# Performance work log

Measured on AMD Instinct MI355X. Metric: run time of the kernel, lower is better.

## Reference

```python
import jax, jax.numpy as jnp
import numpy as np

N = 20000          # skill_num (nodes)
D = 128            # skill_embed_dim
E = 640000         # edges (avg degree 32)
T = 12             # seq_len
L = 3              # gcn_layers
PRESERVE = 0.1     # residual preserve_ratio


def setup_inputs() -> dict:
    key = jax.random.key(0)
    ks = jax.random.split(key, 8)
    demand_seq_emb = jax.random.normal(ks[0], (N, T, D), jnp.float32)
    supply_seq_emb = jax.random.normal(ks[1], (N, T, D), jnp.float32)
    edge_index = jax.random.randint(ks[2], (2, E), 0, N, dtype=jnp.int32)
    edge_attr = jax.random.uniform(ks[3], (E,), jnp.float32)
    emb_weight = jax.random.normal(ks[4], (N, D), jnp.float32) * 0.02
    fuse_W = jax.random.normal(ks[5], (D, 3 * D), jnp.float32) * (1.0 / np.sqrt(3 * D))
    fuse_b = jnp.zeros((D,), jnp.float32)
    gcn_W = jax.random.normal(ks[6], (L, D, D), jnp.float32) * (1.0 / np.sqrt(D))
    gcn_b = jnp.zeros((L, D), jnp.float32)
    return {
        "demand_seq_emb": demand_seq_emb,
        "supply_seq_emb": supply_seq_emb,
        "l": T, "t_s": 0, "t_e": T,                 # unused by forward (placeholders)
        "edge_index": edge_index,
        "edge_attr": edge_attr,
        "comm": 0, "skill_semantic_embed": 0, "init_emb": 0,  # unused placeholders
        "emb_weight": emb_weight,
        "fuse_W": fuse_W, "fuse_b": fuse_b,
        "gcn_W": gcn_W, "gcn_b": gcn_b,
    }


def _gcn_norm(src, dst, edge_w, n):
    """PyG gcn_norm with self-loops: norm_e = d^-1/2[src] * w_e * d^-1/2[dst]."""
    loop = jnp.arange(n, dtype=src.dtype)
    src2 = jnp.concatenate([src, loop])
    dst2 = jnp.concatenate([dst, loop])
    w2 = jnp.concatenate([edge_w, jnp.ones((n,), edge_w.dtype)])
    deg = jax.ops.segment_sum(w2, dst2, num_segments=n)
    dinv = jnp.where(deg > 0, jax.lax.rsqrt(deg), 0.0)
    norm = dinv[src2] * w2 * dinv[dst2]
    return src2, dst2, norm


def reference(demand_seq_emb, supply_seq_emb, l, t_s, t_e, edge_index, edge_attr,
              comm, skill_semantic_embed, init_emb,
              emb_weight, fuse_W, fuse_b, gcn_W, gcn_b):
    # fuse static embedding with last-step demand/supply sequence embeddings
    seq_last = jnp.concatenate([demand_seq_emb[:, -1, :], supply_seq_emb[:, -1, :]], axis=-1)  # [N,2D]
    fused = jnp.concatenate([emb_weight, seq_last], axis=-1) @ fuse_W.T + fuse_b  # [N,D]

    # edges are generated with all indices < skill_num, so the torch-side
    # `(edge_index < skill_num).all(0)` filter is the identity here.
    src, dst = edge_index[0], edge_index[1]
    src2, dst2, norm = _gcn_norm(src, dst, edge_attr, N)

    temp = fused
    for i in range(L):  # small fixed layer count
        x = temp @ gcn_W[i].T                                   # [N,D] linear (bias added post-agg)
        msg = norm[:, None] * x[src2]                           # gather + scale
        out = jax.ops.segment_sum(msg, dst2, num_segments=N) + gcn_b[i]  # scatter-add
        temp = (1.0 - PRESERVE) * out + PRESERVE * temp         # residual blend
    return temp  # skill_embs [N, D]
```

## Files before the change

### kernel.cpp

```cpp
#include <hip/hip_runtime.h>
#include <hip/hip_fp16.h>

#define NN 20000
#define DD 128
#define EE 640000
#define TSEQ 12
#define CAP 128

__device__ __forceinline__ void fma4(float4& acc, float a, const float4& w) {
  acc.x += a * w.x; acc.y += a * w.y; acc.z += a * w.z; acc.w += a * w.w;
}

__device__ __forceinline__ float4 h8_to_f4(uint2 v) {
  union { unsigned u; __half2 h; } a, b;
  a.u = v.x; b.u = v.y;
  float2 fa = __half22float2(a.h);
  float2 fb = __half22float2(b.h);
  return make_float4(fa.x, fa.y, fb.x, fb.y);
}

__device__ __forceinline__ uint2 f4_to_h8(float4 o) {
  union { unsigned u; __half2 h; } a, b;
  a.h = __floats2half2_rn(o.x, o.y);
  b.h = __floats2half2_rn(o.z, o.w);
  uint2 r; r.x = a.u; r.y = b.u;
  return r;
}

__global__ void k_init(float* __restrict__ deg, int* __restrict__ cnt) {
  int i = blockIdx.x * blockDim.x + threadIdx.x;
  if (i < NN) { deg[i] = 1.0f; cnt[i] = 0; }
}

__global__ void k_edge(const int* __restrict__ src, const int* __restrict__ dst,
                       const float* __restrict__ w,
                       float* __restrict__ deg, int* __restrict__ cnt,
                       uint2* __restrict__ csr) {
  int e = blockIdx.x * blockDim.x + threadIdx.x;
  if (e < EE) {
    int s = src[e], d = dst[e];
    float we = w[e];
    atomicAdd(&deg[d], we);
    int slot = atomicAdd(&cnt[d], 1);
    if (slot < CAP) csr[(size_t)d * CAP + slot] = make_uint2((unsigned)s, __float_as_uint(we));
  }
}

__global__ void k_transpose_all(const float* __restrict__ fuse_W,
                                const float* __restrict__ gcn_W,
                                float* __restrict__ fuse_Wt,
                                float* __restrict__ gWt0,
                                __half* __restrict__ gWh) {
  int i = blockIdx.x * blockDim.x + threadIdx.x;
  if (i < 49152) {
    int k = i >> 7, d = i & 127;
    fuse_Wt[i] = fuse_W[d * 384 + k];
  } else if (i < 65536) {
    int j = i - 49152;
    int k = j >> 7, d = j & 127;
    gWt0[j] = gcn_W[d * 128 + k];
  } else if (i < 98304) {
    int j = i - 65536;
    int l = 1 + (j >> 14), jj = j & 16383;
    int k = jj >> 7, d = jj & 127;
    gWh[j] = (__half)gcn_W[l * 16384 + d * 128 + k];
  }
}

#define G_TN 2
#define G_BN 32

__global__ __launch_bounds__(256, 4) void k_gemm(
    const float* __restrict__ a0, int s0,
    const float* __restrict__ a1, int s1,
    const float* __restrict__ a2, int s2,
    int nparts,
    const float* __restrict__ Wt,
    const float* __restrict__ bias,
    const float* __restrict__ deg_pm,
    float* __restrict__ outf,
    uint2* __restrict__ outh)
{
  __shared__ float Ws[64 * 128];
  const int t = threadIdx.x;
  const int dq = t & 15;
  const int ng = t >> 4;
  const int n_base = blockIdx.x * G_BN + ng * G_TN;

  float4 acc0[G_TN], acc1[G_TN];
  #pragma unroll
  for (int i = 0; i < G_TN; ++i) {
    acc0[i] = make_float4(0.f, 0.f, 0.f, 0.f);
    acc1[i] = make_float4(0.f, 0.f, 0.f, 0.f);
  }

  for (int p = 0; p < nparts; ++p) {
    const float* ap; int as;
    if (p == 0) { ap = a0; as = s0; }
    else if (p == 1) { ap = a1; as = s1; }
    else { ap = a2; as = s2; }
    const float* rp[G_TN];
    #pragma unroll
    for (int i = 0; i < G_TN; ++i) {
      int r = n_base + i; if (r >= NN) r = NN - 1;
      rp[i] = ap + (size_t)r * as;
    }

    for (int c = 0; c < 2; ++c) {
      const float4* wsrc = (const float4*)(Wt + (p * 128 + c * 64) * 128);
      float4* wdst = (float4*)Ws;
      #pragma unroll
      for (int it = 0; it < 8; ++it) wdst[it * 256 + t] = wsrc[it * 256 + t];
      __syncthreads();

      const int ks = c * 64;
      for (int k = 0; k < 64; k += 4) {
        float4 av[G_TN];
        #pragma unroll
        for (int i = 0; i < G_TN; ++i) av[i] = *(const float4*)(rp[i] + ks + k);
        #pragma unroll
        for (int j = 0; j < 4; ++j) {
          const float4 w0 = *(const float4*)&Ws[(k + j) * 128 + 4 * dq];
          const float4 w1 = *(const float4*)&Ws[(k + j) * 128 + 64 + 4 * dq];
          #pragma unroll
          for (int i = 0; i < G_TN; ++i) {
            float a = (j == 0) ? av[i].x : (j == 1) ? av[i].y : (j == 2) ? av[i].z : av[i].w;
            fma4(acc0[i], a, w0);
            fma4(acc1[i], a, w1);
          }
        }
      }
      __syncthreads();
    }
  }

  float4 b0 = make_float4(0.f,0.f,0.f,0.f), b1 = b0;
  if (bias) {
    b0 = *(const float4*)&bias[4 * dq];
    b1 = *(const float4*)&bias[64 + 4 * dq];
  }
  #pragma unroll
  for (int i = 0; i < G_TN; ++i) {
    int r = n_base + i;
    if (r < NN) {
      float4 o0 = make_float4(acc0[i].x + b0.x, acc0[i].y + b0.y,
                              acc0[i].z + b0.z, acc0[i].w + b0.w);
      float4 o1 = make_float4(acc1[i].x + b1.x, acc1[i].y + b1.y,
                              acc1[i].z + b1.z, acc1[i].w + b1.w);
      if (outf) {
        *(float4*)(outf + (size_t)r * DD + 4 * dq) = o0;
        *(float4*)(outf + (size_t)r * DD + 64 + 4 * dq) = o1;
      } else {
        float di = rsqrtf(deg_pm[r]);
        o0.x *= di; o0.y *= di; o0.z *= di; o0.w *= di;
        o1.x *= di; o1.y *= di; o1.z *= di; o1.w *= di;
        outh[(size_t)r * 32 + dq] = f4_to_h8(o0);
        outh[(size_t)r * 32 + 16 + dq] = f4_to_h8(o1);
      }
    }
  }
}

template<bool NEXT>
__global__ __launch_bounds__(256, 4) void k_agg_fused(
    const uint2* __restrict__ xh, const float* __restrict__ tin,
    const int* __restrict__ cnt, const uint2* __restrict__ csr,
    const float* __restrict__ deg, const float* __restrict__ bias,
    const uint2* __restrict__ Wh,
    float* __restrict__ tout,
    uint2* __restrict__ xh_out)
{
  __shared__ float rows[NEXT ? 8 * 128 : 8];
  __shared__ uint2 Whs[NEXT ? 4096 : 8];

  const int t = threadIdx.x;
  const int dq = t & 31;
  const int nl = t >> 5;
  const int n = blockIdx.x * 8 + nl;

  uint2 wreg[16];
  if constexpr (NEXT) {
    #pragma unroll
    for (int i = 0; i < 16; ++i) wreg[i] = Wh[i * 256 + t];
  }

  const float di = rsqrtf(deg[n]);
  float4 acc = h8_to_f4(xh[(size_t)n * 32 + dq]);

  const size_t base = (size_t)n * CAP;
  int m = cnt[n]; if (m > CAP) m = CAP;
  int j = 0;
  for (; j + 8 <= m; j += 8) {
    uint2 c[8];
    #pragma unroll
    for (int u = 0; u < 8; ++u) c[u] = csr[base + j + u];
    uint2 v[8];
    #pragma unroll
    for (int u = 0; u < 8; ++u) v[u] = xh[(size_t)c[u].x * 32 + dq];
    #pragma unroll
    for (int u = 0; u < 8; ++u) fma4(acc, __uint_as_float(c[u].y), h8_to_f4(v[u]));
  }
  for (; j < m; ++j) {
    uint2 c = csr[base + j];
    fma4(acc, __uint_as_float(c.y), h8_to_f4(xh[(size_t)c.x * 32 + dq]));
  }

  const float4 b4 = *(const float4*)&bias[4 * dq];
  const float4 ti = ((const float4*)tin)[(size_t)n * 32 + dq];
  float4 o;
  o.x = 0.9f * (di * acc.x + b4.x) + 0.1f * ti.x;
  o.y = 0.9f * (di * acc.y + b4.y) + 0.1f * ti.y;
  o.z = 0.9f * (di * acc.z + b4.z) + 0.1f * ti.z;
  o.w = 0.9f * (di * acc.w + b4.w) + 0.1f * ti.w;
  ((float4*)tout)[(size_t)n * 32 + dq] = o;

  if constexpr (NEXT) {
    #pragma unroll
    for (int i = 0; i < 16; ++i) Whs[i * 256 + t] = wreg[i];
    *(float4*)&rows[nl * 128 + 4 * dq] = o;
    __syncthreads();

    float4 x = make_float4(0.f, 0.f, 0.f, 0.f);
    const float* myrow = &rows[nl * 128];
    #pragma unroll 4
    for (int k = 0; k < 128; ++k) {
      fma4(x, myrow[k], h8_to_f4(Whs[k * 32 + dq]));
    }
    x.x *= di; x.y *= di; x.z *= di; x.w *= di;
    xh_out[(size_t)n * 32 + dq] = f4_to_h8(x);
  }
}

extern "C" void kernel_launch(void* const* d_in, const int* in_sizes, int n_in,
                              void* d_out, int out_size, void* d_ws, size_t ws_size,
                              hipStream_t stream) {
  const float* demand = (const float*)d_in[0];
  const float* supply = (const float*)d_in[1];
  const int*   eidx   = (const int*)d_in[5];
  const float* eattr  = (const float*)d_in[6];
  const float* emb    = (const float*)d_in[10];
  const float* fuse_W = (const float*)d_in[11];
  const float* fuse_b = (const float*)d_in[12];
  const float* gcn_W  = (const float*)d_in[13];
  const float* gcn_b  = (const float*)d_in[14];
  float* outp = (float*)d_out;

  char* ws = (char*)d_ws;
  size_t o = 0;
  auto alloc = [&](size_t bytes) {
    char* p = ws + o;
    o += (bytes + 255) & ~(size_t)255;
    return p;
  };
  float*  deg     = (float*)alloc((size_t)NN * 4);
  int*    cnt     = (int*)alloc((size_t)NN * 4);
  uint2*  csr     = (uint2*)alloc((size_t)NN * CAP * 8);
  float*  fuse_Wt = (float*)alloc((size_t)384 * 128 * 4);
  float*  gWt0    = (float*)alloc((size_t)128 * 128 * 4);
  __half* gWh     = (__half*)alloc((size_t)2 * 128 * 128 * 2);
  float*  temp0   = (float*)alloc((size_t)NN * DD * 4);
  float*  temp1   = (float*)alloc((size_t)NN * DD * 4);
  uint2*  xh_a    = (uint2*)alloc((size_t)NN * DD * 2);
  uint2*  xh_b    = (uint2*)alloc((size_t)NN * DD * 2);

  const int* srcv = eidx;
  const int* dstv = eidx + EE;

  const int NB = (NN + 255) / 256;
  const int EB = (EE + 255) / 256;

  k_init<<<NB, 256, 0, stream>>>(deg, cnt);
  k_edge<<<EB, 256, 0, stream>>>(srcv, dstv, eattr, deg, cnt, csr);
  k_transpose_all<<<384, 256, 0, stream>>>(fuse_W, gcn_W, fuse_Wt, gWt0, gWh);

  const int GB = (NN + G_BN - 1) / G_BN;
  k_gemm<<<GB, 256, 0, stream>>>(emb, 128,
                                 demand + 11 * 128, TSEQ * 128,
                                 supply + 11 * 128, TSEQ * 128,
                                 3, fuse_Wt, fuse_b, nullptr, temp0, nullptr);
  k_gemm<<<GB, 256, 0, stream>>>(temp0, 128, temp0, 128, temp0, 128,
                                 1, gWt0, nullptr, deg, nullptr, xh_a);

  const int AB = NN / 8;
  k_agg_fused<true ><<<AB, 256, 0, stream>>>(xh_a, temp0, cnt, csr, deg, gcn_b,
                                             (const uint2*)gWh, temp1, xh_b);
  k_agg_fused<true ><<<AB, 256, 0, stream>>>(xh_b, temp1, cnt, csr, deg, gcn_b + 128,
                                             (const uint2*)(gWh + 16384), temp0, xh_a);
  k_agg_fused<false><<<AB, 256, 0, stream>>>(xh_a, temp0, cnt, csr, deg, gcn_b + 256,
                                             nullptr, outp, nullptr);
}
```

Measured before the change: 460.7 us.

## Merge prep kernels, co-schedule edge build with fuse GEMM, pad atomic counters

Init and weight transpose are merged into one prep kernel. The edge-scatter/CSR build now runs in the same launch as the fuse GEMM, split by block index, so the atomic edge work overlaps the compute. The deg and cnt counters are padded to 128-byte strides to cut atomic contention on shared cache lines, and the aggregation unroll grows to 16 with a 4-wide tail. In exchange the padded counters use more memory and are read with strided loads, and the GEMM row clamp is removed because 20000 divides evenly by 32.

```diff
diff --git a/kernel.cpp b/kernel.cpp
--- a/kernel.cpp
+++ b/kernel.cpp
@@ -6,6 +6,7 @@
 #define EE 640000
 #define TSEQ 12
 #define CAP 128
+#define PADI 32
 
 __device__ __forceinline__ void fma4(float4& acc, float a, const float4& w) {
   acc.x += a * w.x; acc.y += a * w.y; acc.z += a * w.z; acc.w += a * w.w;
@@ -27,65 +28,51 @@
   return r;
 }
 
-__global__ void k_init(float* __restrict__ deg, int* __restrict__ cnt) {
-  int i = blockIdx.x * blockDim.x + threadIdx.x;
-  if (i < NN) { deg[i] = 1.0f; cnt[i] = 0; }
-}
-
-__global__ void k_edge(const int* __restrict__ src, const int* __restrict__ dst,
-                       const float* __restrict__ w,
-                       float* __restrict__ deg, int* __restrict__ cnt,
-                       uint2* __restrict__ csr) {
-  int e = blockIdx.x * blockDim.x + threadIdx.x;
-  if (e < EE) {
-    int s = src[e], d = dst[e];
-    float we = w[e];
-    atomicAdd(&deg[d], we);
-    int slot = atomicAdd(&cnt[d], 1);
-    if (slot < CAP) csr[(size_t)d * CAP + slot] = make_uint2((unsigned)s, __float_as_uint(we));
-  }
-}
-
-__global__ void k_transpose_all(const float* __restrict__ fuse_W,
-                                const float* __restrict__ gcn_W,
-                                float* __restrict__ fuse_Wt,
-                                float* __restrict__ gWt0,
-                                __half* __restrict__ gWh) {
-  int i = blockIdx.x * blockDim.x + threadIdx.x;
-  if (i < 49152) {
-    int k = i >> 7, d = i & 127;
-    fuse_Wt[i] = fuse_W[d * 384 + k];
-  } else if (i < 65536) {
-    int j = i - 49152;
-    int k = j >> 7, d = j & 127;
-    gWt0[j] = gcn_W[d * 128 + k];
-  } else if (i < 98304) {
-    int j = i - 65536;
-    int l = 1 + (j >> 14), jj = j & 16383;
-    int k = jj >> 7, d = jj & 127;
-    gWh[j] = (__half)gcn_W[l * 16384 + d * 128 + k];
+__global__ void k_prep(const float* __restrict__ fuse_W,
+                       const float* __restrict__ gcn_W,
+                       float* __restrict__ deg_pad, int* __restrict__ cnt_pad,
+                       float* __restrict__ fuse_Wt,
+                       float* __restrict__ gWt0,
+                       __half* __restrict__ gWh) {
+  int b = blockIdx.x;
+  if (b < 625) {
+    int i = b * 256 + threadIdx.x;
+    float4 z = make_float4((i & 7) == 0 ? 1.0f : 0.0f, 0.f, 0.f, 0.f);
+    ((float4*)deg_pad)[i] = z;
+  } else if (b < 1250) {
+    int i = (b - 625) * 256 + threadIdx.x;
+    ((int4*)cnt_pad)[i] = make_int4(0, 0, 0, 0);
+  } else {
+    int i = (b - 1250) * 256 + threadIdx.x;
+    if (i < 49152) {
+      int k = i >> 7, d = i & 127;
+      fuse_Wt[i] = fuse_W[d * 384 + k];
+    } else if (i < 65536) {
+      int j = i - 49152;
+      int k = j >> 7, d = j & 127;
+      gWt0[j] = gcn_W[d * 128 + k];
+    } else if (i < 98304) {
+      int j = i - 65536;
+      int l = 1 + (j >> 14), jj = j & 16383;
+      int k = jj >> 7, d = jj & 127;
+      gWh[j] = (__half)gcn_W[l * 16384 + d * 128 + k];
+    }
   }
 }
 
 #define G_TN 2
 #define G_BN 32
 
-__global__ __launch_bounds__(256, 4) void k_gemm(
-    const float* __restrict__ a0, int s0,
-    const float* __restrict__ a1, int s1,
-    const float* __restrict__ a2, int s2,
-    int nparts,
-    const float* __restrict__ Wt,
-    const float* __restrict__ bias,
-    const float* __restrict__ deg_pm,
-    float* __restrict__ outf,
-    uint2* __restrict__ outh)
+__device__ __forceinline__ void gemm_body(
+    float* Ws, int gb,
+    const float* a0, int s0, const float* a1, int s1, const float* a2, int s2,
+    int nparts, const float* Wt, const float* bias, const float* deg_pad,
+    float* outf, uint2* outh)
 {
-  __shared__ float Ws[64 * 128];
   const int t = threadIdx.x;
   const int dq = t & 15;
   const int ng = t >> 4;
-  const int n_base = blockIdx.x * G_BN + ng * G_TN;
+  const int n_base = gb * G_BN + ng * G_TN;
 
   float4 acc0[G_TN], acc1[G_TN];
   #pragma unroll
@@ -101,10 +88,7 @@
     else { ap = a2; as = s2; }
     const float* rp[G_TN];
     #pragma unroll
-    for (int i = 0; i < G_TN; ++i) {
-      int r = n_base + i; if (r >= NN) r = NN - 1;
-      rp[i] = ap + (size_t)r * as;
-    }
+    for (int i = 0; i < G_TN; ++i) rp[i] = ap + (size_t)(n_base + i) * as;
 
     for (int c = 0; c < 2; ++c) {
       const float4* wsrc = (const float4*)(Wt + (p * 128 + c * 64) * 128);
@@ -142,30 +126,62 @@
   #pragma unroll
   for (int i = 0; i < G_TN; ++i) {
     int r = n_base + i;
-    if (r < NN) {
-      float4 o0 = make_float4(acc0[i].x + b0.x, acc0[i].y + b0.y,
-                              acc0[i].z + b0.z, acc0[i].w + b0.w);
-      float4 o1 = make_float4(acc1[i].x + b1.x, acc1[i].y + b1.y,
-                              acc1[i].z + b1.z, acc1[i].w + b1.w);
-      if (outf) {
-        *(float4*)(outf + (size_t)r * DD + 4 * dq) = o0;
-        *(float4*)(outf + (size_t)r * DD + 64 + 4 * dq) = o1;
-      } else {
-        float di = rsqrtf(deg_pm[r]);
-        o0.x *= di; o0.y *= di; o0.z *= di; o0.w *= di;
-        o1.x *= di; o1.y *= di; o1.z *= di; o1.w *= di;
-        outh[(size_t)r * 32 + dq] = f4_to_h8(o0);
-        outh[(size_t)r * 32 + 16 + dq] = f4_to_h8(o1);
-      }
+    float4 o0 = make_float4(acc0[i].x + b0.x, acc0[i].y + b0.y,
+                            acc0[i].z + b0.z, acc0[i].w + b0.w);
+    float4 o1 = make_float4(acc1[i].x + b1.x, acc1[i].y + b1.y,
+                            acc1[i].z + b1.z, acc1[i].w + b1.w);
+    if (outf) {
+      *(float4*)(outf + (size_t)r * DD + 4 * dq) = o0;
+      *(float4*)(outf + (size_t)r * DD + 64 + 4 * dq) = o1;
+    } else {
+      float di = rsqrtf(deg_pad[(size_t)r * PADI]);
+      o0.x *= di; o0.y *= di; o0.z *= di; o0.w *= di;
+      o1.x *= di; o1.y *= di; o1.z *= di; o1.w *= di;
+      outh[(size_t)r * 32 + dq] = f4_to_h8(o0);
+      outh[(size_t)r * 32 + 16 + dq] = f4_to_h8(o1);
     }
   }
+}
+
+__global__ __launch_bounds__(256, 4) void k_mega(
+    const float* __restrict__ emb, const float* __restrict__ demand,
+    const float* __restrict__ supply,
+    const float* __restrict__ fuse_Wt, const float* __restrict__ fuse_b,
+    float* __restrict__ temp0,
+    const int* __restrict__ src, const int* __restrict__ dst,
+    const float* __restrict__ w,
+    float* __restrict__ deg_pad, int* __restrict__ cnt_pad,
+    uint2* __restrict__ csr)
+{
+  __shared__ float Ws[64 * 128];
+  if (blockIdx.x < 625) {
+    gemm_body(Ws, blockIdx.x,
+              emb, 128, demand + 11 * 128, TSEQ * 128, supply + 11 * 128, TSEQ * 128,
+              3, fuse_Wt, fuse_b, nullptr, temp0, nullptr);
+  } else {
+    int e = (blockIdx.x - 625) * 256 + threadIdx.x;
+    int s = src[e], d = dst[e];
+    float we = w[e];
+    atomicAdd(&deg_pad[(size_t)d * PADI], we);
+    int slot = atomicAdd(&cnt_pad[(size_t)d * PADI], 1);
+    if (slot < CAP) csr[(size_t)d * CAP + slot] = make_uint2((unsigned)s, __float_as_uint(we));
+  }
+}
+
+__global__ __launch_bounds__(256, 4) void k_gemm_x0(
+    const float* __restrict__ temp0, const float* __restrict__ gWt0,
+    const float* __restrict__ deg_pad, uint2* __restrict__ outh)
+{
+  __shared__ float Ws[64 * 128];
+  gemm_body(Ws, blockIdx.x, temp0, 128, temp0, 128, temp0, 128,
+            1, gWt0, nullptr, deg_pad, nullptr, outh);
 }
 
 template<bool NEXT>
 __global__ __launch_bounds__(256, 4) void k_agg_fused(
     const uint2* __restrict__ xh, const float* __restrict__ tin,
-    const int* __restrict__ cnt, const uint2* __restrict__ csr,
-    const float* __restrict__ deg, const float* __restrict__ bias,
+    const int* __restrict__ cnt_pad, const uint2* __restrict__ csr,
+    const float* __restrict__ deg_pad, const float* __restrict__ bias,
     const uint2* __restrict__ Wh,
     float* __restrict__ tout,
     uint2* __restrict__ xh_out)
@@ -184,21 +200,31 @@
     for (int i = 0; i < 16; ++i) wreg[i] = Wh[i * 256 + t];
   }
 
-  const float di = rsqrtf(deg[n]);
+  const float di = rsqrtf(deg_pad[(size_t)n * PADI]);
   float4 acc = h8_to_f4(xh[(size_t)n * 32 + dq]);
 
   const size_t base = (size_t)n * CAP;
-  int m = cnt[n]; if (m > CAP) m = CAP;
+  int m = cnt_pad[(size_t)n * PADI]; if (m > CAP) m = CAP;
   int j = 0;
-  for (; j + 8 <= m; j += 8) {
-    uint2 c[8];
-    #pragma unroll
-    for (int u = 0; u < 8; ++u) c[u] = csr[base + j + u];
-    uint2 v[8];
-    #pragma unroll
-    for (int u = 0; u < 8; ++u) v[u] = xh[(size_t)c[u].x * 32 + dq];
-    #pragma unroll
-    for (int u = 0; u < 8; ++u) fma4(acc, __uint_as_float(c[u].y), h8_to_f4(v[u]));
+  for (; j + 16 <= m; j += 16) {
+    uint2 c[16];
+    #pragma unroll
+    for (int u = 0; u < 16; ++u) c[u] = csr[base + j + u];
+    uint2 v[16];
+    #pragma unroll
+    for (int u = 0; u < 16; ++u) v[u] = xh[(size_t)c[u].x * 32 + dq];
+    #pragma unroll
+    for (int u = 0; u < 16; ++u) fma4(acc, __uint_as_float(c[u].y), h8_to_f4(v[u]));
+  }
+  for (; j + 4 <= m; j += 4) {
+    uint2 c[4];
+    #pragma unroll
+    for (int u = 0; u < 4; ++u) c[u] = csr[base + j + u];
+    uint2 v[4];
+    #pragma unroll
+    for (int u = 0; u < 4; ++u) v[u] = xh[(size_t)c[u].x * 32 + dq];
+    #pragma unroll
+    for (int u = 0; u < 4; ++u) fma4(acc, __uint_as_float(c[u].y), h8_to_f4(v[u]));
   }
   for (; j < m; ++j) {
     uint2 c = csr[base + j];
@@ -252,8 +278,8 @@
     o += (bytes + 255) & ~(size_t)255;
     return p;
   };
-  float*  deg     = (float*)alloc((size_t)NN * 4);
-  int*    cnt     = (int*)alloc((size_t)NN * 4);
+  float*  deg_pad = (float*)alloc((size_t)NN * PADI * 4);
+  int*    cnt_pad = (int*)alloc((size_t)NN * PADI * 4);
   uint2*  csr     = (uint2*)alloc((size_t)NN * CAP * 8);
   float*  fuse_Wt = (float*)alloc((size_t)384 * 128 * 4);
   float*  gWt0    = (float*)alloc((size_t)128 * 128 * 4);
@@ -266,26 +292,18 @@
   const int* srcv = eidx;
   const int* dstv = eidx + EE;
 
-  const int NB = (NN + 255) / 256;
-  const int EB = (EE + 255) / 256;
-
-  k_init<<<NB, 256, 0, stream>>>(deg, cnt);
-  k_edge<<<EB, 256, 0, stream>>>(srcv, dstv, eattr, deg, cnt, csr);
-  k_transpose_all<<<384, 256, 0, stream>>>(fuse_W, gcn_W, fuse_Wt, gWt0, gWh);
-
-  const int GB = (NN + G_BN - 1) / G_BN;
-  k_gemm<<<GB, 256, 0, stream>>>(emb, 128,
-                                 demand + 11 * 128, TSEQ * 128,
-                                 supply + 11 * 128, TSEQ * 128,
-                                 3, fuse_Wt, fuse_b, nullptr, temp0, nullptr);
-  k_gemm<<<GB, 256, 0, stream>>>(temp0, 128, temp0, 128, temp0, 128,
-                                 1, gWt0, nullptr, deg, nullptr, xh_a);
+  k_prep<<<1634, 256, 0, stream>>>(fuse_W, gcn_W, deg_pad, cnt_pad, fuse_Wt, gWt0, gWh);
+
+  k_mega<<<3125, 256, 0, stream>>>(emb, demand, supply, fuse_Wt, fuse_b, temp0,
+                                   srcv, dstv, eattr, deg_pad, cnt_pad, csr);
+
+  k_gemm_x0<<<625, 256, 0, stream>>>(temp0, gWt0, deg_pad, xh_a);
 
   const int AB = NN / 8;
-  k_agg_fused<true ><<<AB, 256, 0, stream>>>(xh_a, temp0, cnt, csr, deg, gcn_b,
+  k_agg_fused<true ><<<AB, 256, 0, stream>>>(xh_a, temp0, cnt_pad, csr, deg_pad, gcn_b,
                                              (const uint2*)gWh, temp1, xh_b);
-  k_agg_fused<true ><<<AB, 256, 0, stream>>>(xh_b, temp1, cnt, csr, deg, gcn_b + 128,
+  k_agg_fused<true ><<<AB, 256, 0, stream>>>(xh_b, temp1, cnt_pad, csr, deg_pad, gcn_b + 128,
                                              (const uint2*)(gWh + 16384), temp0, xh_a);
-  k_agg_fused<false><<<AB, 256, 0, stream>>>(xh_a, temp0, cnt, csr, deg, gcn_b + 256,
+  k_agg_fused<false><<<AB, 256, 0, stream>>>(xh_a, temp0, cnt_pad, csr, deg_pad, gcn_b + 256,
                                              nullptr, outp, nullptr);
 }
```

Result: faster. 427.8 us (-7.2%).
